# Optimization experiments

Measured on AMD Instinct MI355X. Metric: run time of the kernel, lower is better.

Reference implementation:

```python
import jax, jax.numpy as jnp
import numpy as np

H = 8  # num_heads

def layernorm(x, g, b, eps=1e-5):
    mu = jnp.mean(x, axis=-1, keepdims=True)
    var = jnp.var(x, axis=-1, keepdims=True)
    return (x - mu) * jax.lax.rsqrt(var + eps) * g + b

def mha(x, w_in, b_in, w_out, b_out, bias=None):
    # x: [B_, S, D]; w_in: [3D, D] packed q,k,v (PyTorch MHA layout)
    B_, S, D = x.shape
    hd = D // H
    qkv = x @ w_in.T + b_in                      # [B_, S, 3D]
    q, k, v = jnp.split(qkv, 3, axis=-1)
    def heads(t):
        return t.reshape(B_, S, H, hd).transpose(0, 2, 1, 3)  # [B_, H, S, hd]
    q, k, v = heads(q), heads(k), heads(v)
    scores = jnp.einsum('bhqd,bhkd->bhqk', q, k) / jnp.sqrt(jnp.float32(hd))
    if bias is not None:
        scores = scores + bias[None, None]        # broadcast [S,S] bias
    attn = jax.nn.softmax(scores, axis=-1)
    out = jnp.einsum('bhqk,bhkd->bhqd', attn, v)  # [B_, H, S, hd]
    out = out.transpose(0, 2, 1, 3).reshape(B_, S, D)
    return out @ w_out.T + b_out

def setup_inputs() -> dict:
    key = jax.random.key(0)
    ks = jax.random.split(key, 8)
    B, T, N, D, F = 32, 12, 325, 128, 512
    s = 0.05
    return {
        'x': jax.random.normal(ks[0], (B, T, N, D), jnp.float32),
        't_w_in': jax.random.normal(ks[1], (3 * D, D), jnp.float32) * s,
        't_b_in': jnp.zeros((3 * D,), jnp.float32),
        't_w_out': jax.random.normal(ks[2], (D, D), jnp.float32) * s,
        't_b_out': jnp.zeros((D,), jnp.float32),
        's_w_in': jax.random.normal(ks[3], (3 * D, D), jnp.float32) * s,
        's_b_in': jnp.zeros((3 * D,), jnp.float32),
        's_w_out': jax.random.normal(ks[4], (D, D), jnp.float32) * s,
        's_b_out': jnp.zeros((D,), jnp.float32),
        'g_bias': jax.random.normal(ks[5], (N, N), jnp.float32) * 0.5,
        'norm_t_g': jnp.ones((D,), jnp.float32),
        'norm_t_b': jnp.zeros((D,), jnp.float32),
        'norm_s_g': jnp.ones((D,), jnp.float32),
        'norm_s_b': jnp.zeros((D,), jnp.float32),
        'ff_w1': jax.random.normal(ks[6], (F, D), jnp.float32) * s,
        'ff_b1': jnp.zeros((F,), jnp.float32),
        'ff_w2': jax.random.normal(ks[7], (D, F), jnp.float32) * s,
        'ff_b2': jnp.zeros((D,), jnp.float32),
        'norm_ff_g': jnp.ones((D,), jnp.float32),
        'norm_ff_b': jnp.zeros((D,), jnp.float32),
    }

def reference(x, t_w_in, t_b_in, t_w_out, t_b_out, s_w_in, s_b_in, s_w_out, s_b_out,
              g_bias, norm_t_g, norm_t_b, norm_s_g, norm_s_b,
              ff_w1, ff_b1, ff_w2, ff_b2, norm_ff_g, norm_ff_b):
    B, T, N, D = x.shape
    # Temporal attention: each sensor attends over time
    xt = x.transpose(0, 2, 1, 3).reshape(B * N, T, D)
    xt = mha(xt, t_w_in, t_b_in, t_w_out, t_b_out)
    x = layernorm(x + xt.reshape(B, N, T, D).transpose(0, 2, 1, 3), norm_t_g, norm_t_b)
    # Spatial attention with graph bias: each timestep attends over sensors
    xs = x.reshape(B * T, N, D)
    xs = mha(xs, s_w_in, s_b_in, s_w_out, s_b_out, bias=g_bias)
    x = layernorm(x + xs.reshape(B, T, N, D), norm_s_g, norm_s_b)
    # FFN
    h = jax.nn.gelu(x @ ff_w1.T + ff_b1) @ ff_w2.T + ff_b2
    x = layernorm(x + h, norm_ff_g, norm_ff_b)
    return x
```

## Files before the change

### kernel.cpp

```cpp
#include <hip/hip_runtime.h>
#include <cstdint>
#include <cstddef>


#define B_ 32
#define T_ 12
#define N_ 325
#define D_ 128
#define H_ 8
#define F_ 512
#define NT 124800
#define BCH 8
#define CHK (BCH * T_ * N_)
#define NCHUNK 4
#define GT ((CHK + 63) / 64)
#define NKT 11
#define NQT 21
#define QSPLIT 3
#define QPG 7
#define GBS 328

#define O_XBF 0UL
#define O_Y1B 31948800UL
#define O_QKV 63897600UL
#define O_ABUF 87859200UL
#define O_WB 95846400UL
#define O_PB 96370688UL

typedef __attribute__((ext_vector_type(8))) short bf16x8;
typedef __attribute__((ext_vector_type(4))) short bf16x4;
typedef __attribute__((ext_vector_type(4))) float f32x4;
typedef __attribute__((ext_vector_type(2))) unsigned int u32x2;
typedef __attribute__((ext_vector_type(4))) unsigned int u32x4;

#define SCL 0.36067376022224085f

#if __has_builtin(__builtin_amdgcn_exp2f)
#define EXP2(x) __builtin_amdgcn_exp2f(x)
#else
#define EXP2(x) __expf((x) * 0.6931471805599453f)
#endif

__device__ inline float b2f(unsigned short b) {
  unsigned int u = ((unsigned int)b) << 16;
  return __builtin_bit_cast(float, u);
}
__device__ inline unsigned short f2b(float f) {
  unsigned int u = __builtin_bit_cast(unsigned int, f);
  unsigned int r = (u + 0x7FFFu + ((u >> 16) & 1u)) >> 16;
  return (unsigned short)r;
}
__device__ inline unsigned short f2b_fast(float f) {
  unsigned int u = __builtin_bit_cast(unsigned int, f);
  return (unsigned short)((u + 0x8000u) >> 16);
}
__device__ inline f32x4 mfma16(bf16x8 a, bf16x8 b, f32x4 c) {
  return __builtin_amdgcn_mfma_f32_16x16x32_bf16(a, b, c, 0, 0, 0);
}
#if __has_builtin(__builtin_amdgcn_mfma_f32_16x16x16bf16_1k)
__device__ inline f32x4 mfma16k16(bf16x4 a, bf16x4 b, f32x4 c) {
  return __builtin_amdgcn_mfma_f32_16x16x16bf16_1k(a, b, c, 0, 0, 0);
}
#else
__device__ inline f32x4 mfma16k16(bf16x4 a, bf16x4 b, f32x4 c) {
  f32x4 d;
  asm volatile("s_nop 3\n\t"
               "v_mfma_f32_16x16x16_bf16 %0, %1, %2, %3\n\t"
               "s_nop 7\n\ts_nop 7"
               : "=&v"(d)
               : "v"(a), "v"(b), "v"(c));
  return d;
}
#endif
__device__ inline bf16x8 cat44(bf16x4 a, bf16x4 b) {
  u32x2 ua = __builtin_bit_cast(u32x2, a);
  u32x2 ub = __builtin_bit_cast(u32x2, b);
  u32x4 u = {ua.x, ua.y, ub.x, ub.y};
  return __builtin_bit_cast(bf16x8, u);
}
__device__ inline float gelu_t(float x) {
  float x3 = x * x * x;
  return 0.5f * x * (1.0f + tanhf(0.7978845608f * (x + 0.044715f * x3)));
}

__global__ void k_convert8(const void* __restrict__ src,
                           unsigned short* __restrict__ dB, long n8,
                           const unsigned short* __restrict__ probe) {
  long i = (long)blockIdx.x * blockDim.x + threadIdx.x;
  if (i >= n8) return;
  if (probe[0] != 0) {
    ((uint4*)dB)[i] = ((const uint4*)src)[i];
  } else {
    float4 a = ((const float4*)src)[i * 2];
    float4 b = ((const float4*)src)[i * 2 + 1];
    uint4 o;
    unsigned short* op = (unsigned short*)&o;
    op[0] = f2b(a.x); op[1] = f2b(a.y); op[2] = f2b(a.z); op[3] = f2b(a.w);
    op[4] = f2b(b.x); op[5] = f2b(b.y); op[6] = f2b(b.z); op[7] = f2b(b.w);
    ((uint4*)dB)[i] = o;
  }
}

__global__ void k_conv_params(
    const void* s1, const void* s2, const void* s3, const void* s4,
    const void* s5, const void* s6, const void* s7, const void* s8,
    const void* s9, const void* s10, const void* s11, const void* s12,
    const void* s13, const void* s14, const void* s15, const void* s16,
    const void* s17, const void* s18, const void* s19, char* ws,
    const unsigned short* __restrict__ probe) {
  long i = (long)blockIdx.x * blockDim.x + threadIdx.x;
  bool isbf = probe[0] != 0;
  long o = 0;
#define LOADV(src, j) \
  (isbf ? b2f(((const unsigned short*)(src))[j]) : ((const float*)(src))[j])
#define SEGB(src, dstoff, n)                                        \
  if (i < o + (n)) {                                                \
    long j = i - o;                                                 \
    ((unsigned short*)(ws + (dstoff)))[j] = f2b(LOADV(src, j));     \
    return;                                                         \
  }                                                                 \
  o += (n);
#define SEGF(src, dstoff, n)                              \
  if (i < o + (n)) {                                      \
    long j = i - o;                                       \
    ((float*)(ws + (dstoff)))[j] = LOADV(src, j);         \
    return;                                               \
  }                                                       \
  o += (n);
  SEGB(s1, O_WB + 0, 49152)
  SEGF(s2, O_PB + 0, 384)
  SEGB(s3, O_WB + 98304, 16384)
  SEGF(s4, O_PB + 1536, 128)
  SEGB(s5, O_WB + 131072, 49152)
  SEGF(s6, O_PB + 2048, 384)
  SEGB(s7, O_WB + 229376, 16384)
  SEGF(s8, O_PB + 3584, 128)
  if (i < o + 326 * GBS) {
    long j = i - o;
    int q = (int)(j / GBS);
    int s = (int)(j - (long)q * GBS);
    float v = (q < 325 && s < 325) ? LOADV(s9, (long)q * 325 + s) * 1.44269504f
                                   : 0.0f;
    ((float*)(ws + O_PB + 9728))[j] = v;
    return;
  }
  o += 326 * GBS;
  SEGF(s10, O_PB + 6656, 128)
  SEGF(s11, O_PB + 7168, 128)
  SEGF(s12, O_PB + 7680, 128)
  SEGF(s13, O_PB + 8192, 128)
  SEGB(s14, O_WB + 262144, 65536)
  SEGF(s15, O_PB + 4096, 512)
  SEGB(s16, O_WB + 393216, 65536)
  SEGF(s17, O_PB + 6144, 128)
  SEGF(s18, O_PB + 8704, 128)
  SEGF(s19, O_PB + 9216, 128)
#undef SEGB
#undef SEGF
#undef LOADV
}
#define CONVP_TOTAL 371504L

template <int ROWS, int KTOT>
__device__ inline void stage_tile(short (*dst)[ROWS][32],
                                  const unsigned short* __restrict__ src,
                                  int row0, int k0, int tid, int Mrows) {
  constexpr int CH = ROWS * 16;
#pragma unroll
  for (int it = 0; it < CH / 256; ++it) {
    int cb = tid + it * 256;
    int row = cb >> 4;
    int kc = cb & 15;
    int gr = row0 + row;
    gr = gr < Mrows ? gr : Mrows - 1;
    uint4 v = *(const uint4*)(src + (size_t)gr * KTOT + (size_t)k0 + kc * 8);
    *(uint4*)(&dst[kc >> 2][row][(kc & 3) * 8]) = v;
  }
}

template <int KTOT, bool GELU>
__global__ __launch_bounds__(256) void k_gemm_store(
    const unsigned short* __restrict__ Ab, const unsigned short* __restrict__ Wb,
    const float* __restrict__ bias, unsigned short* __restrict__ outB, int Ntot,
    int Mrows, int Nrows) {
  __shared__ __align__(16) union USm {
    struct { short A[4][64][32]; short B[4][64][32]; } s;
    float C[64][68];
  } sm;
  const int tid = threadIdx.x;
  const int m0 = blockIdx.x * 64;
  const int n0 = blockIdx.y * 64;
  const int lane = tid & 63, wave = tid >> 6;
  const int wm = wave >> 1, wn = wave & 1;
  const int ml = lane & 15, quad = lane >> 4;
  f32x4 acc[2][2] = {};
#pragma unroll
  for (int c = 0; c < KTOT / 128; ++c) {
    if (c) __syncthreads();
    stage_tile<64, KTOT>(sm.s.A, Ab, m0, c * 128, tid, Mrows);
    stage_tile<64, KTOT>(sm.s.B, Wb, n0, c * 128, tid, Nrows);
    __syncthreads();
#pragma unroll
    for (int kc = 0; kc < 4; ++kc) {
      bf16x8 a0 = *(const bf16x8*)&sm.s.A[kc][wm * 32 + ml][quad * 8];
      bf16x8 a1 = *(const bf16x8*)&sm.s.A[kc][wm * 32 + 16 + ml][quad * 8];
      bf16x8 b0 = *(const bf16x8*)&sm.s.B[kc][wn * 32 + ml][quad * 8];
      bf16x8 b1 = *(const bf16x8*)&sm.s.B[kc][wn * 32 + 16 + ml][quad * 8];
      acc[0][0] = mfma16(a0, b0, acc[0][0]);
      acc[0][1] = mfma16(a0, b1, acc[0][1]);
      acc[1][0] = mfma16(a1, b0, acc[1][0]);
      acc[1][1] = mfma16(a1, b1, acc[1][1]);
    }
  }
  __syncthreads();
#pragma unroll
  for (int mi = 0; mi < 2; ++mi)
#pragma unroll
    for (int ni = 0; ni < 2; ++ni)
#pragma unroll
      for (int r = 0; r < 4; ++r)
        sm.C[wm * 32 + mi * 16 + quad * 4 + r][wn * 32 + ni * 16 + ml] =
            acc[mi][ni][r];
  __syncthreads();
  const int trow = tid >> 4;
  const int tcol = (tid & 15) * 4;
  const float4 bv = *(const float4*)&bias[n0 + tcol];
#pragma unroll
  for (int it = 0; it < 4; ++it) {
    int row = it * 16 + trow;
    int gm = m0 + row;
    float4 cv = *(const float4*)&sm.C[row][tcol];
    float v0 = cv.x + bv.x, v1 = cv.y + bv.y, v2 = cv.z + bv.z,
          v3 = cv.w + bv.w;
    if (GELU) {
      v0 = gelu_t(v0); v1 = gelu_t(v1); v2 = gelu_t(v2); v3 = gelu_t(v3);
    }
    if (gm < Mrows) {
      ushort4 ov;
      ov.x = f2b(v0); ov.y = f2b(v1); ov.z = f2b(v2); ov.w = f2b(v3);
      *(ushort4*)&outB[(size_t)gm * Ntot + n0 + tcol] = ov;
    }
  }
}

template <int KTOT, bool FINAL>
__global__ __launch_bounds__(256) void k_gemm_ln(
    const unsigned short* __restrict__ Ab, const unsigned short* __restrict__ Wb,
    const float* __restrict__ bias, const unsigned short* __restrict__ resid,
    const float* __restrict__ gamma, const float* __restrict__ beta,
    unsigned short* __restrict__ outB, void* __restrict__ dOut, size_t row0g,
    const unsigned short* __restrict__ probe, int Mrows) {
  __shared__ __align__(16) union USm {
    struct { short A[4][64][32]; short B[4][128][32]; } s;
    float C[64][132];
  } sm;
  const int tid = threadIdx.x;
  const int m0 = blockIdx.x * 64;
  const int lane = tid & 63, wave = tid >> 6;
  const int wm = wave >> 1, wn = wave & 1;
  const int ml = lane & 15, quad = lane >> 4;
  f32x4 acc[2][4] = {};
#pragma unroll
  for (int c = 0; c < KTOT / 128; ++c) {
    if (c) __syncthreads();
    stage_tile<64, KTOT>(sm.s.A, Ab, m0, c * 128, tid, Mrows);
    stage_tile<128, KTOT>(sm.s.B, Wb, 0, c * 128, tid, 128);
    __syncthreads();
#pragma unroll
    for (int kc = 0; kc < 4; ++kc) {
      bf16x8 a[2], b[4];
#pragma unroll
      for (int mi = 0; mi < 2; ++mi)
        a[mi] = *(const bf16x8*)&sm.s.A[kc][wm * 32 + mi * 16 + ml][quad * 8];
#pragma unroll
      for (int ni = 0; ni < 4; ++ni)
        b[ni] = *(const bf16x8*)&sm.s.B[kc][wn * 64 + ni * 16 + ml][quad * 8];
#pragma unroll
      for (int mi = 0; mi < 2; ++mi)
#pragma unroll
        for (int ni = 0; ni < 4; ++ni)
          acc[mi][ni] = mfma16(a[mi], b[ni], acc[mi][ni]);
    }
  }
  __syncthreads();
#pragma unroll
  for (int mi = 0; mi < 2; ++mi)
#pragma unroll
    for (int ni = 0; ni < 4; ++ni)
#pragma unroll
      for (int r = 0; r < 4; ++r)
        sm.C[wm * 32 + mi * 16 + quad * 4 + r][wn * 64 + ni * 16 + ml] =
            acc[mi][ni][r];
  __syncthreads();
  const int c0 = lane * 2;
  const float bia0 = bias[c0], bia1 = bias[c0 + 1];
  const float ga0 = gamma[c0], ga1 = gamma[c0 + 1];
  const float be0 = beta[c0], be1 = beta[c0 + 1];
  const bool isbf = FINAL ? (probe[0] != 0) : true;
#pragma unroll
  for (int rr = 0; rr < 16; ++rr) {
    int row = wave * 16 + rr;
    int gm = m0 + row;
    bool valid = gm < Mrows;
    float2 cc = *(const float2*)&sm.C[row][c0];
    float r0 = 0.f, r1 = 0.f;
    if (valid) {
      ushort2 rv = *(const ushort2*)&resid[(size_t)gm * 128 + c0];
      r0 = b2f(rv.x);
      r1 = b2f(rv.y);
    }
    float v0 = cc.x + bia0 + r0, v1 = cc.y + bia1 + r1;
    float s = v0 + v1, q = v0 * v0 + v1 * v1;
#pragma unroll
    for (int off = 1; off < 64; off <<= 1) {
      s += __shfl_xor(s, off);
      q += __shfl_xor(q, off);
    }
    float mean = s * (1.f / 128.f);
    float var = q * (1.f / 128.f) - mean * mean;
    float rs = rsqrtf(var + 1e-5f);
    float y0 = (v0 - mean) * rs * ga0 + be0;
    float y1 = (v1 - mean) * rs * ga1 + be1;
    if (valid) {
      if (FINAL) {
        if (isbf) {
          ushort2 ov; ov.x = f2b(y0); ov.y = f2b(y1);
          *(ushort2*)((unsigned short*)dOut + (row0g + gm) * 128 + c0) = ov;
        } else {
          float2 ov; ov.x = y0; ov.y = y1;
          *(float2*)((float*)dOut + (row0g + gm) * 128 + c0) = ov;
        }
      } else {
        ushort2 ov; ov.x = f2b(y0); ov.y = f2b(y1);
        *(ushort2*)&outB[(size_t)gm * 128 + c0] = ov;
      }
    }
  }
}

__global__ __launch_bounds__(128) void k_attn_t(
    const unsigned short* __restrict__ qkv, unsigned short* __restrict__ A) {
  __shared__ float ls[12][384];
  const int tid = threadIdx.x;
  const int bx = blockIdx.x;
  const int b = bx / N_, n = bx % N_;
  for (int i = tid; i < 576; i += 128) {
    int t = i / 48, c = (i % 48) * 8;
    size_t tok = (size_t)(b * T_ + t) * N_ + n;
    uint4 v = *(const uint4*)(qkv + tok * 384 + c);
    const unsigned short* pv = (const unsigned short*)&v;
    float4 f0 = {b2f(pv[0]), b2f(pv[1]), b2f(pv[2]), b2f(pv[3])};
    float4 f1 = {b2f(pv[4]), b2f(pv[5]), b2f(pv[6]), b2f(pv[7])};
    *(float4*)&ls[t][c] = f0;
    *(float4*)&ls[t][c + 4] = f1;
  }
  __syncthreads();
  if (tid < 96) {
    int h = tid / 12, q = tid % 12;
    const float* qv = &ls[q][h * 16];
    float s[12];
    float m = -1e30f;
#pragma unroll
    for (int t = 0; t < 12; ++t) {
      float d = 0.f;
#pragma unroll
      for (int dd = 0; dd < 16; ++dd) d += qv[dd] * ls[t][128 + h * 16 + dd];
      s[t] = d * 0.25f;
      m = fmaxf(m, s[t]);
    }
    float l = 0.f;
#pragma unroll
    for (int t = 0; t < 12; ++t) {
      s[t] = __expf(s[t] - m);
      l += s[t];
    }
    float inv = 1.0f / l;
    float o[16];
#pragma unroll
    for (int dd = 0; dd < 16; ++dd) {
      float acc = 0.f;
#pragma unroll
      for (int t = 0; t < 12; ++t) acc += s[t] * ls[t][256 + h * 16 + dd];
      o[dd] = acc * inv;
    }
    size_t otok = (size_t)(b * T_ + q) * N_ + n;
#pragma unroll
    for (int g = 0; g < 4; ++g) {
      ushort4 ov;
      ov.x = f2b(o[g * 4 + 0]); ov.y = f2b(o[g * 4 + 1]);
      ov.z = f2b(o[g * 4 + 2]); ov.w = f2b(o[g * 4 + 3]);
      *(ushort4*)&A[otok * 128 + h * 16 + g * 4] = ov;
    }
  }
}

__global__ __launch_bounds__(256) void k_attn_s(
    const unsigned short* __restrict__ qkv, const float* __restrict__ gbp,
    unsigned short* __restrict__ A) {
  __shared__ short Ks[352 * 24];
  __shared__ short Vt[16 * 364];
  const int tid = threadIdx.x;
  const int bt = blockIdx.x, h = blockIdx.y, qs = blockIdx.z;
  const size_t base = (size_t)bt * N_;
  for (int i = tid; i < 352 * 2; i += 256) {
    int s = i >> 1, half = i & 1;
    if (s < N_) {
      size_t rb = (base + s) * 384 + h * 16 + half * 8;
      uint4 kv = *(const uint4*)(qkv + rb + 128);
      *(uint4*)&Ks[s * 24 + half * 8] = kv;
      uint4 vv = *(const uint4*)(qkv + rb + 256);
      const unsigned short* vs = (const unsigned short*)&vv;
#pragma unroll
      for (int e = 0; e < 8; ++e) Vt[(half * 8 + e) * 364 + s] = vs[e];
    } else {
      *(uint4*)&Ks[s * 24 + half * 8] = uint4{0, 0, 0, 0};
#pragma unroll
      for (int e = 0; e < 8; ++e) Vt[(half * 8 + e) * 364 + s] = 0;
    }
  }
  __syncthreads();
  const int lane = tid & 63, wave = tid >> 6;
  const int ml = lane & 15, quad = lane >> 4;
  const f32x4 fz = {0.f, 0.f, 0.f, 0.f};
  const bf16x8 ones8 = {16256, 16256, 16256, 16256,
                        16256, 16256, 16256, 16256};
  const int qt0 = qs * QPG;
  const int qtA = qt0 + wave;
  const bool hasB = wave < 3;
  const int qtB = hasB ? qtA + 4 : qtA;
  const int qA = qtA * 16 + ml, qB = qtB * 16 + ml;
  const int qcA = qA < N_ ? qA : N_ - 1;
  const int qcB = qB < N_ ? qB : N_ - 1;
  const bf16x4 qfA =
      *(const bf16x4*)(qkv + (base + qcA) * 384 + h * 16 + quad * 4);
  const bf16x4 qfB =
      *(const bf16x4*)(qkv + (base + qcB) * 384 + h * 16 + quad * 4);
  const float* gbA = gbp + (size_t)qcA * GBS;
  const float* gbB = gbp + (size_t)qcB * GBS;
  f32x4 OA = fz, OB = fz, LA = fz, LB = fz;
  for (int kt = 0; kt < NKT; ++kt) {
    const int sb = kt * 32;
    bf16x4 k0f = *(const bf16x4*)&Ks[(sb + ml) * 24 + quad * 4];
    bf16x4 k1f = *(const bf16x4*)&Ks[(sb + 16 + ml) * 24 + quad * 4];
    f32x4 S0A = mfma16k16(k0f, qfA, fz);
    f32x4 S1A = mfma16k16(k1f, qfA, fz);
    f32x4 S0B = mfma16k16(k0f, qfB, fz);
    f32x4 S1B = mfma16k16(k1f, qfB, fz);
    const int sb1 = (sb + 16 <= 312) ? sb + 16 : 312;
    float4 g0A = *(const float4*)&gbA[sb + quad * 4];
    float4 g1A = *(const float4*)&gbA[sb1 + quad * 4];
    float4 g0B = *(const float4*)&gbB[sb + quad * 4];
    float4 g1B = *(const float4*)&gbB[sb1 + quad * 4];
    float p0A[4], p1A[4], p0B[4], p1B[4];
#define EXPV(p, S, g)                      \
  p[0] = EXP2(fmaf(S[0], SCL, g.x));       \
  p[1] = EXP2(fmaf(S[1], SCL, g.y));       \
  p[2] = EXP2(fmaf(S[2], SCL, g.z));       \
  p[3] = EXP2(fmaf(S[3], SCL, g.w));
    EXPV(p0A, S0A, g0A)
    EXPV(p1A, S1A, g1A)
    EXPV(p0B, S0B, g0B)
    EXPV(p1B, S1B, g1B)
#undef EXPV
    if (kt == NKT - 1) {
#pragma unroll
      for (int r = 0; r < 4; ++r) {
        if (sb + quad * 4 + r >= N_) { p0A[r] = 0.f; p0B[r] = 0.f; }
        p1A[r] = 0.f;
        p1B[r] = 0.f;
      }
    }
    bf16x4 a0A = {(short)f2b_fast(p0A[0]), (short)f2b_fast(p0A[1]),
                  (short)f2b_fast(p0A[2]), (short)f2b_fast(p0A[3])};
    bf16x4 a1A = {(short)f2b_fast(p1A[0]), (short)f2b_fast(p1A[1]),
                  (short)f2b_fast(p1A[2]), (short)f2b_fast(p1A[3])};
    bf16x4 a0B = {(short)f2b_fast(p0B[0]), (short)f2b_fast(p0B[1]),
                  (short)f2b_fast(p0B[2]), (short)f2b_fast(p0B[3])};
    bf16x4 a1B = {(short)f2b_fast(p1B[0]), (short)f2b_fast(p1B[1]),
                  (short)f2b_fast(p1B[2]), (short)f2b_fast(p1B[3])};
    bf16x4 v0 = *(const bf16x4*)&Vt[ml * 364 + sb + quad * 4];
    bf16x4 v1 = *(const bf16x4*)&Vt[ml * 364 + sb + 16 + quad * 4];
    OA = mfma16k16(a0A, v0, OA);
    OA = mfma16k16(a1A, v1, OA);
    OB = mfma16k16(a0B, v0, OB);
    OB = mfma16k16(a1B, v1, OB);
    LA = mfma16(cat44(a0A, a1A), ones8, LA);
    LB = mfma16(cat44(a0B, a1B), ones8, LB);
  }
#pragma unroll
  for (int r = 0; r < 4; ++r) {
    int qg = qtA * 16 + quad * 4 + r;
    if (qg < N_)
      A[(base + qg) * 128 + h * 16 + ml] = f2b(OA[r] / LA[r]);
  }
  if (hasB) {
#pragma unroll
    for (int r = 0; r < 4; ++r) {
      int qg = qtB * 16 + quad * 4 + r;
      if (qg < N_)
        A[(base + qg) * 128 + h * 16 + ml] = f2b(OB[r] / LB[r]);
    }
  }
}

extern "C" void kernel_launch(void* const* d_in, const int* in_sizes, int n_in,
                              void* d_out, int out_size, void* d_ws,
                              size_t ws_size, hipStream_t stream) {
  char* ws = (char*)d_ws;
  const unsigned short* probe = (const unsigned short*)d_in[10];

  unsigned short* xbf = (unsigned short*)(ws + O_XBF);
  unsigned short* y1b = (unsigned short*)(ws + O_Y1B);
  unsigned short* qkvc = (unsigned short*)(ws + O_QKV);
  unsigned short* Abufc = (unsigned short*)(ws + O_ABUF);
  unsigned short* hbuf = qkvc;
  unsigned short* y2b = xbf;
  char* wb = ws + O_WB;
  unsigned short* wt_in = (unsigned short*)(wb + 0);
  unsigned short* wt_out = (unsigned short*)(wb + 98304);
  unsigned short* wsp_in = (unsigned short*)(wb + 131072);
  unsigned short* wsp_out = (unsigned short*)(wb + 229376);
  unsigned short* wff1 = (unsigned short*)(wb + 262144);
  unsigned short* wff2 = (unsigned short*)(wb + 393216);
  char* pb = ws + O_PB;
  float* p_t_b_in = (float*)(pb + 0);
  float* p_t_b_out = (float*)(pb + 1536);
  float* p_s_b_in = (float*)(pb + 2048);
  float* p_s_b_out = (float*)(pb + 3584);
  float* p_ff_b1 = (float*)(pb + 4096);
  float* p_ff_b2 = (float*)(pb + 6144);
  float* p_ntg = (float*)(pb + 6656);
  float* p_ntb = (float*)(pb + 7168);
  float* p_nsg = (float*)(pb + 7680);
  float* p_nsb = (float*)(pb + 8192);
  float* p_nfg = (float*)(pb + 8704);
  float* p_nfb = (float*)(pb + 9216);
  float* p_gbp = (float*)(pb + 9728);

  {
    long n8 = (long)NT * 128 / 8;
    k_convert8<<<dim3((unsigned)((n8 + 255) / 256)), dim3(256), 0, stream>>>(
        d_in[0], xbf, n8, probe);
    k_conv_params<<<dim3((unsigned)((CONVP_TOTAL + 255) / 256)), dim3(256), 0,
                    stream>>>(d_in[1], d_in[2], d_in[3], d_in[4], d_in[5],
                              d_in[6], d_in[7], d_in[8], d_in[9], d_in[10],
                              d_in[11], d_in[12], d_in[13], d_in[14], d_in[15],
                              d_in[16], d_in[17], d_in[18], d_in[19], ws,
                              probe);
  }

  dim3 blk(256);
  for (int c = 0; c < NCHUNK; ++c) {
    size_t tok0 = (size_t)c * CHK;
    k_gemm_store<128, false><<<dim3(GT, 6), blk, 0, stream>>>(
        xbf + tok0 * 128, wt_in, p_t_b_in, qkvc, 384, CHK, 384);
    k_attn_t<<<dim3(BCH * N_), dim3(128), 0, stream>>>(qkvc, Abufc);
    k_gemm_ln<128, false><<<dim3(GT), blk, 0, stream>>>(
        Abufc, wt_out, p_t_b_out, xbf + tok0 * 128, p_ntg, p_ntb,
        y1b + tok0 * 128, nullptr, 0, probe, CHK);
  }
  for (int c = 0; c < NCHUNK; ++c) {
    size_t tok0 = (size_t)c * CHK;
    k_gemm_store<128, false><<<dim3(GT, 6), blk, 0, stream>>>(
        y1b + tok0 * 128, wsp_in, p_s_b_in, qkvc, 384, CHK, 384);
    k_attn_s<<<dim3(BCH * T_, H_, QSPLIT), blk, 0, stream>>>(qkvc, p_gbp,
                                                             Abufc);
    k_gemm_ln<128, false><<<dim3(GT), blk, 0, stream>>>(
        Abufc, wsp_out, p_s_b_out, y1b + tok0 * 128, p_nsg, p_nsb,
        y2b + tok0 * 128, nullptr, 0, probe, CHK);
  }
  for (int c = 0; c < NCHUNK; ++c) {
    size_t tok0 = (size_t)c * CHK;
    k_gemm_store<128, true><<<dim3(GT, 8), blk, 0, stream>>>(
        y2b + tok0 * 128, wff1, p_ff_b1, hbuf, 512, CHK, 512);
    k_gemm_ln<512, true><<<dim3(GT), blk, 0, stream>>>(
        hbuf, wff2, p_ff_b2, y2b + tok0 * 128, p_nfg, p_nfb, nullptr, d_out,
        tok0, probe, CHK);
  }
}
```

Measured before the change: 731.7 us.

## Stage GEMM tiles with direct global-to-LDS loads and fast GELU tanh

New measurement: 712.9 us. -2.6%, faster.

```diff
diff --git a/kernel.cpp b/kernel.cpp
--- a/kernel.cpp
+++ b/kernel.cpp
@@ -79,9 +79,24 @@
   return __builtin_bit_cast(bf16x8, u);
 }
 __device__ inline float gelu_t(float x) {
-  float x3 = x * x * x;
-  return 0.5f * x * (1.0f + tanhf(0.7978845608f * (x + 0.044715f * x3)));
-}
+  float z = 0.7978845608f * (x + 0.044715f * x * x * x);
+  float e = EXP2(-2.885390082f * fabsf(z));
+  float t = (1.0f - e) * __builtin_amdgcn_rcpf(1.0f + e);
+  t = copysignf(t, z);
+  return 0.5f * x * (1.0f + t);
+}
+
+#define GLD16(gsrc, ldst)                                      \
+  __builtin_amdgcn_global_load_lds(                            \
+      (__attribute__((address_space(1))) void*)(gsrc),         \
+      (__attribute__((address_space(3))) void*)(ldst), 16, 0, 0)
+
+#define STAGE_FENCE()                                    \
+  do {                                                   \
+    asm volatile("s_waitcnt vmcnt(0)" ::: "memory");     \
+    __builtin_amdgcn_sched_barrier(0);                   \
+    __syncthreads();                                     \
+  } while (0)
 
 __global__ void k_convert8(const void* __restrict__ src,
                            unsigned short* __restrict__ dB, long n8,
@@ -162,19 +177,27 @@
 #define CONVP_TOTAL 371504L
 
 template <int ROWS, int KTOT>
-__device__ inline void stage_tile(short (*dst)[ROWS][32],
-                                  const unsigned short* __restrict__ src,
-                                  int row0, int k0, int tid, int Mrows) {
-  constexpr int CH = ROWS * 16;
-#pragma unroll
-  for (int it = 0; it < CH / 256; ++it) {
-    int cb = tid + it * 256;
-    int row = cb >> 4;
-    int kc = cb & 15;
+__device__ inline void stage_tile_async(short (*dst)[ROWS][32],
+                                        const unsigned short* __restrict__ src,
+                                        int row0, int k0, int tid, int Mrows) {
+  static_assert(ROWS == 64 || ROWS == 128, "pow2 rows");
+  constexpr int LOG2R = (ROWS == 64) ? 6 : 7;
+  const int lane = tid & 63;
+  const int wave = tid >> 6;
+  short* base = &dst[0][0][0];
+#pragma unroll
+  for (int it = 0; it < ROWS / 16; ++it) {
+    const int cbase = (it * 4 + wave) * 64;
+    const int c = cbase + lane;
+    const int sub = c & 3;
+    const int t = c >> 2;
+    const int row = t & (ROWS - 1);
+    const int slice = t >> LOG2R;
+    const int kc = slice * 4 + sub;
     int gr = row0 + row;
     gr = gr < Mrows ? gr : Mrows - 1;
-    uint4 v = *(const uint4*)(src + (size_t)gr * KTOT + (size_t)k0 + kc * 8);
-    *(uint4*)(&dst[kc >> 2][row][(kc & 3) * 8]) = v;
+    const unsigned short* g = src + (size_t)gr * KTOT + (size_t)k0 + kc * 8;
+    GLD16(g, base + (size_t)cbase * 8);
   }
 }
 
@@ -197,9 +220,9 @@
 #pragma unroll
   for (int c = 0; c < KTOT / 128; ++c) {
     if (c) __syncthreads();
-    stage_tile<64, KTOT>(sm.s.A, Ab, m0, c * 128, tid, Mrows);
-    stage_tile<64, KTOT>(sm.s.B, Wb, n0, c * 128, tid, Nrows);
-    __syncthreads();
+    stage_tile_async<64, KTOT>(sm.s.A, Ab, m0, c * 128, tid, Mrows);
+    stage_tile_async<64, KTOT>(sm.s.B, Wb, n0, c * 128, tid, Nrows);
+    STAGE_FENCE();
 #pragma unroll
     for (int kc = 0; kc < 4; ++kc) {
       bf16x8 a0 = *(const bf16x8*)&sm.s.A[kc][wm * 32 + ml][quad * 8];
@@ -263,9 +286,9 @@
 #pragma unroll
   for (int c = 0; c < KTOT / 128; ++c) {
     if (c) __syncthreads();
-    stage_tile<64, KTOT>(sm.s.A, Ab, m0, c * 128, tid, Mrows);
-    stage_tile<128, KTOT>(sm.s.B, Wb, 0, c * 128, tid, 128);
-    __syncthreads();
+    stage_tile_async<64, KTOT>(sm.s.A, Ab, m0, c * 128, tid, Mrows);
+    stage_tile_async<128, KTOT>(sm.s.B, Wb, 0, c * 128, tid, 128);
+    STAGE_FENCE();
 #pragma unroll
     for (int kc = 0; kc < 4; ++kc) {
       bf16x8 a[2], b[4];
```
